# Performance work log

Hardware: AMD Instinct MI355X
Metric: run time of the kernel (lower is better)

Reference implementation:

```python
import jax, jax.numpy as jnp
import numpy as np
from jax import lax

V, E, H, T = 50000, 256, 512, 16  # vocab, embed_dim, hidden_dim, num_tags
B, S = 32, 512
C = 128          # conv channels
HD = H // 2      # per-direction LSTM hidden


def setup_inputs() -> dict:
    key = jax.random.key(0)
    ks = jax.random.split(key, 20)
    g = lambda k, shape, s=0.05: jax.random.normal(k, shape, jnp.float32) * s
    return {
        "x": jax.random.randint(ks[0], (B, S), 0, V),
        "mask": jnp.ones((B, S), jnp.int32),
        "tags": jax.random.randint(ks[1], (B, S), 0, T),
        "embed_table": g(ks[2], (V, E), 0.1),
        "conv_w": g(ks[3], (C, E, 3)),
        "conv_b": g(ks[4], (C,)),
        "wih_f": g(ks[5], (4 * HD, C)),
        "whh_f": g(ks[6], (4 * HD, HD)),
        "bih_f": g(ks[7], (4 * HD,)),
        "bhh_f": g(ks[8], (4 * HD,)),
        "wih_b": g(ks[9], (4 * HD, C)),
        "whh_b": g(ks[10], (4 * HD, HD)),
        "bih_b": g(ks[11], (4 * HD,)),
        "bhh_b": g(ks[12], (4 * HD,)),
        "fc_w": g(ks[13], (T, H)),
        "fc_b": g(ks[14], (T,)),
        "start_trans": g(ks[15], (T,), 0.1),
        "end_trans": g(ks[16], (T,), 0.1),
        "trans": g(ks[17], (T, T), 0.1),
    }


def _lstm_dir(xs, wih, whh, bih, bhh, reverse):
    # xs: [S, B, D] -> hidden states [S, B, HD], PyTorch gate order i,f,g,o
    b = xs.shape[1]
    h0 = jnp.zeros((b, whh.shape[1]), xs.dtype)

    def step(carry, xt):
        h, c = carry
        gates = xt @ wih.T + h @ whh.T + bih + bhh  # [B, 4*HD]
        i, f, g, o = jnp.split(gates, 4, axis=-1)
        c = jax.nn.sigmoid(f) * c + jax.nn.sigmoid(i) * jnp.tanh(g)
        h = jax.nn.sigmoid(o) * jnp.tanh(c)
        return (h, c), h

    _, hs = lax.scan(step, (h0, h0), xs, reverse=reverse)
    return hs


def _crf_nll(emissions, tg, m, start_trans, end_trans, trans):
    # emissions [S,B,T], tg [S,B] int, m [S,B] float -> per-seq -loglik mean
    bidx = jnp.arange(emissions.shape[1])
    # numerator: score of the gold path
    score = start_trans[tg[0]] + emissions[0, bidx, tg[0]]

    def num_step(s, inp):
        prev_t, cur_t, em, mi = inp
        return s + (trans[prev_t, cur_t] + em[bidx, cur_t]) * mi, None

    score, _ = lax.scan(num_step, score, (tg[:-1], tg[1:], emissions[1:], m[1:]))
    seq_ends = m.sum(0).astype(jnp.int32) - 1
    score = score + end_trans[tg[seq_ends, bidx]]
    # denominator: forward algorithm (log partition)
    alpha = start_trans + emissions[0]  # [B,T]

    def den_step(a, inp):
        em, mi = inp
        nxt = jax.nn.logsumexp(a[:, :, None] + trans[None] + em[:, None, :], axis=1)
        return jnp.where(mi[:, None] > 0, nxt, a), None

    alpha, _ = lax.scan(den_step, alpha, (emissions[1:], m[1:]))
    logz = jax.nn.logsumexp(alpha + end_trans[None], axis=1)
    return -jnp.mean(score - logz)


def reference(x, mask, tags, embed_table, conv_w, conv_b, wih_f, whh_f, bih_f,
              bhh_f, wih_b, whh_b, bih_b, bhh_b, fc_w, fc_b, start_trans,
              end_trans, trans):
    emb = embed_table[x]                       # [B,S,E]
    xc = jnp.transpose(emb, (0, 2, 1))         # [B,E,S]
    conv = lax.conv_general_dilated(xc, conv_w, (1,), [(1, 1)],
                                    dimension_numbers=("NCH", "OIH", "NCH"))
    feat = jax.nn.relu(conv + conv_b[None, :, None])   # [B,C,S]
    xs = jnp.transpose(feat, (2, 0, 1))        # [S,B,C]
    hf = _lstm_dir(xs, wih_f, whh_f, bih_f, bhh_f, False)
    hb = _lstm_dir(xs, wih_b, whh_b, bih_b, bhh_b, True)
    h = jnp.concatenate([hf, hb], axis=-1)     # [S,B,H]
    emissions = h @ fc_w.T + fc_b              # [S,B,T]
    m = jnp.transpose(mask, (1, 0)).astype(emissions.dtype)
    tg = jnp.transpose(tags, (1, 0))
    return _crf_nll(emissions, tg, m, start_trans, end_trans, trans)
```

## Files before the change

### kernel.cpp

```cpp
#include <hip/hip_runtime.h>
#include <hip/hip_bf16.h>

constexpr int NB = 32, NS = 512, NE = 256, NC = 128, NHD = 256, NG = 1024, NT = 16, NH = 512;

typedef float f32x4 __attribute__((ext_vector_type(4)));
typedef short bf16x8 __attribute__((ext_vector_type(8)));

__device__ __forceinline__ unsigned short f2bf(float f) {
    unsigned u = __float_as_uint(f);
    u += 0x7fffu + ((u >> 16) & 1u);
    return (unsigned short)(u >> 16);
}
__device__ __forceinline__ float bf2f(unsigned short s) {
    return __uint_as_float(((unsigned)s) << 16);
}
__device__ __forceinline__ float vexp2(float x) {
    float r; asm("v_exp_f32 %0, %1" : "=v"(r) : "v"(x)); return r;
}
__device__ __forceinline__ float vrcp(float x) {
    float r; asm("v_rcp_f32 %0, %1" : "=v"(r) : "v"(x)); return r;
}
__device__ __forceinline__ float vlog2(float x) {
    float r; asm("v_log_f32 %0, %1" : "=v"(r) : "v"(x)); return r;
}
__device__ __forceinline__ unsigned char f2fp8(float v) {
    int r = __builtin_amdgcn_cvt_pk_fp8_f32(v, 0.f, 0, false);
    return (unsigned char)(r & 0xff);
}
__device__ __constant__ float KSC[4] = {-1.442695041f, -1.442695041f, 2.885390082f, -1.442695041f};

__global__ void k_prep_convw(const float* __restrict__ w, float* __restrict__ wT) {
    int i = blockIdx.x * 256 + threadIdx.x;
    if (i >= 768 * 128) return;
    int e3 = i >> 7, c = i & 127;
    wT[i] = w[c * 768 + e3];
}

__global__ void k_prep_scale(const float* __restrict__ whh_f, const float* __restrict__ whh_b,
                             float* __restrict__ scale) {
    int d = blockIdx.y;
    const float* src = d ? whh_b : whh_f;
    int col = blockIdx.x * 256 + threadIdx.x;
    if (col >= 1024) return;
    int j = col >> 2, g = col & 3;
    const float* p = src + (size_t)(g * 256 + j) * 256;
    float m = 0.f;
    for (int k = 0; k < 256; ++k) m = fmaxf(m, fabsf(p[k]));
    scale[d * 1024 + col] = (m > 0.f) ? (m * (1.f / 448.f)) : 1.f;
}

__global__ void k_prep_whh_frag8(const float* __restrict__ whh_f, const float* __restrict__ whh_b,
                                 const float* __restrict__ scale, unsigned char* __restrict__ whhF8) {
    int i = blockIdx.x * 256 + threadIdx.x;
    if (i >= (1 << 19)) return;
    int e = i & 7;
    int lane = (i >> 3) & 63;
    int g = (i >> 9) & 3;
    int kt = (i >> 11) & 7;
    int w = (i >> 14) & 15;
    int d = (i >> 18) & 1;
    const float* src = d ? whh_b : whh_f;
    int j = w * 16 + (lane & 15);
    int k = kt * 32 + (lane >> 4) * 8 + e;
    float sc = scale[d * 1024 + j * 4 + g];
    float v = src[(g * 256 + j) * 256 + k] / sc;
    whhF8[i] = f2fp8(v);
}

__global__ void k_prep_wih_frag(const float* __restrict__ wih_f, const float* __restrict__ wih_b,
                                unsigned short* __restrict__ wihF) {
    int i = blockIdx.x * 256 + threadIdx.x;
    if (i >= (1 << 18)) return;
    int e = i & 7;
    int lane = (i >> 3) & 63;
    int kt = (i >> 9) & 3;
    int ctg = (i >> 11) & 63;
    int d = (i >> 17) & 1;
    const float* src = d ? wih_b : wih_f;
    int row = lane & 15;
    int cell = ctg * 4 + (row >> 2), g = row & 3;
    int k = kt * 32 + (lane >> 4) * 8 + e;
    wihF[i] = f2bf(src[(g * 256 + cell) * 128 + k] * KSC[g]);
}

__global__ void k_prep_bias(const float* __restrict__ bih_f, const float* __restrict__ bhh_f,
                            const float* __restrict__ bih_b, const float* __restrict__ bhh_b,
                            float* __restrict__ bias2s) {
    int d = blockIdx.y;
    const float* bi = d ? bih_b : bih_f;
    const float* bh = d ? bhh_b : bhh_f;
    int i = blockIdx.x * 256 + threadIdx.x;
    if (i >= NG) return;
    int g = i & 3, j = i >> 2;
    bias2s[(size_t)d * NG + i] = (bi[g * 256 + j] + bh[g * 256 + j]) * KSC[g];
}

__global__ __launch_bounds__(128) void k_conv(const int* __restrict__ x,
                                              const float* __restrict__ table,
                                              const float* __restrict__ wT,
                                              const float* __restrict__ conv_b,
                                              unsigned short* __restrict__ feat) {
    int b = blockIdx.y;
    int s0 = blockIdx.x * 8;
    int c = threadIdx.x;
    __shared__ float win[10][NE];
    for (int i = 0; i < 10; ++i) {
        int s = s0 - 1 + i;
        if (s < 0 || s >= NS) {
            for (int e = c; e < NE; e += 128) win[i][e] = 0.f;
        } else {
            int tok = x[b * NS + s];
            const float* row = table + (size_t)tok * NE;
            for (int e = c; e < NE; e += 128) win[i][e] = row[e];
        }
    }
    __syncthreads();
    float acc[8];
    float bc = conv_b[c];
#pragma unroll
    for (int p = 0; p < 8; ++p) acc[p] = bc;
    for (int e = 0; e < NE; ++e) {
        float r[10];
#pragma unroll
        for (int i = 0; i < 10; ++i) r[i] = win[i][e];
#pragma unroll
        for (int k = 0; k < 3; ++k) {
            float wv = wT[(e * 3 + k) * NC + c];
#pragma unroll
            for (int p = 0; p < 8; ++p) acc[p] += wv * r[p + k];
        }
    }
#pragma unroll
    for (int p = 0; p < 8; ++p) {
        feat[((size_t)b * NS + s0 + p) * NC + c] = f2bf(fmaxf(acc[p], 0.f));
    }
}

__global__ __launch_bounds__(256) void k_xgate(const unsigned short* __restrict__ feat,
                                               const unsigned short* __restrict__ wihF,
                                               const float* __restrict__ bias2s,
                                               unsigned short* __restrict__ xg) {
    int d = blockIdx.y;
    int p0 = blockIdx.x * 16;
    int tid = threadIdx.x;
    int w = tid >> 6, l = tid & 63;
    int l15 = l & 15, lq = l >> 4;
    int p = p0 + l15, b = p & 31, s = p >> 5;
    const unsigned short* fp = feat + ((size_t)b * NS + s) * NC + lq * 8;
    bf16x8 bf[4];
#pragma unroll
    for (int kt = 0; kt < 4; ++kt) bf[kt] = *(const bf16x8*)(fp + kt * 32);
    const unsigned short* WF = wihF + ((size_t)d << 17);
    unsigned short* XGD = xg + (size_t)d * NS * NB * NG;
#pragma unroll
    for (int ct = 0; ct < 16; ++ct) {
        int ctg = w * 16 + ct;
        int cell = ctg * 4 + lq;
        float4 bv = *(const float4*)(bias2s + (size_t)d * NG + cell * 4);
        f32x4 acc = {bv.x, bv.y, bv.z, bv.w};
#pragma unroll
        for (int kt = 0; kt < 4; ++kt) {
            bf16x8 af = *(const bf16x8*)(WF + (((size_t)ctg * 4 + kt) * 64 + l) * 8);
            acc = __builtin_amdgcn_mfma_f32_16x16x32_bf16(af, bf[kt], acc, 0, 0, 0);
        }
        unsigned long long hp = (unsigned long long)f2bf(acc[0])
                              | ((unsigned long long)f2bf(acc[1]) << 16)
                              | ((unsigned long long)f2bf(acc[2]) << 32)
                              | ((unsigned long long)f2bf(acc[3]) << 48);
        *(unsigned long long*)(XGD + (size_t)p * 1024 + cell * 4) = hp;
    }
}

__global__ __launch_bounds__(1024, 1) void k_lstm2(const unsigned char* __restrict__ whhF8,
                                                   const float* __restrict__ scale,
                                                   const unsigned short* __restrict__ xg,
                                                   unsigned short* __restrict__ hcat) {
    int bid = blockIdx.x;
    int d = bid >> 1, bh = bid & 1;
    int tid = threadIdx.x;
    int w = tid >> 6, l = tid & 63;
    int l15 = l & 15, lq = l >> 4;
    __shared__ unsigned char hbuf[2][16][280];
    for (int i = tid; i < 2 * 16 * 280; i += 1024) (&hbuf[0][0][0])[i] = 0;
    unsigned long long wf[32];
    const unsigned char* wp = whhF8 + ((size_t)(d * 16 + w) << 14) + (size_t)l * 8;
#pragma unroll
    for (int f = 0; f < 32; ++f) wf[f] = *(const unsigned long long*)(wp + f * 512);
    int cell = w * 16 + l15;
    float csc[4];
#pragma unroll
    for (int g = 0; g < 4; ++g)
        csc[g] = scale[d * 1024 + cell * 4 + g] * KSC[g];
    const unsigned short* XG = xg + (size_t)d * NS * NB * NG;
    float cst[4] = {};
    __syncthreads();
    int cur = 0;
    unsigned long long xq[4];
    {
        int s0 = d ? (NS - 1) : 0;
#pragma unroll
        for (int r = 0; r < 4; ++r)
            xq[r] = *(const unsigned long long*)(
                XG + (size_t)(s0 * 32 + bh * 16 + lq * 4 + r) * 1024 + cell * 4);
    }
    for (int step = 0; step < NS; ++step) {
        int s = d ? (NS - 1 - step) : step;
        unsigned long long xn[4];
        {
            int stn = (step + 1 < NS) ? step + 1 : step;
            int sn = d ? (NS - 1 - stn) : stn;
#pragma unroll
            for (int r = 0; r < 4; ++r)
                xn[r] = *(const unsigned long long*)(
                    XG + (size_t)(sn * 32 + bh * 16 + lq * 4 + r) * 1024 + cell * 4);
        }
        f32x4 acc[4];
#pragma unroll
        for (int g = 0; g < 4; ++g) acc[g] = (f32x4){0.f, 0.f, 0.f, 0.f};
#pragma unroll
        for (int kt = 0; kt < 8; ++kt) {
            unsigned long long a = *(const unsigned long long*)&hbuf[cur][l15][kt * 32 + lq * 8];
#pragma unroll
            for (int g = 0; g < 4; ++g)
                acc[g] = __builtin_amdgcn_mfma_f32_16x16x32_fp8_fp8(
                    (long long)a, (long long)wf[kt * 4 + g], acc[g], 0, 0, 0);
        }
        int nxt = cur ^ 1;
#pragma unroll
        for (int r = 0; r < 4; ++r) {
            unsigned long long xv = xq[r];
            float pi = fmaf(acc[0][r], csc[0], bf2f((unsigned short)xv));
            float pf = fmaf(acc[1][r], csc[1], bf2f((unsigned short)(xv >> 16)));
            float pg = fmaf(acc[2][r], csc[2], bf2f((unsigned short)(xv >> 32)));
            float po = fmaf(acc[3][r], csc[3], bf2f((unsigned short)(xv >> 48)));
            float si = vrcp(1.f + vexp2(pi));
            float sf = vrcp(1.f + vexp2(pf));
            float tg = fmaf(-2.f, vrcp(1.f + vexp2(pg)), 1.f);
            float so = vrcp(1.f + vexp2(po));
            float c = fmaf(sf, cst[r], si * tg);
            cst[r] = c;
            float tc = fmaf(-2.f, vrcp(1.f + vexp2(2.885390082f * c)), 1.f);
            float h = so * tc;
            int b = lq * 4 + r;
            __builtin_nontemporal_store(f2bf(h),
                hcat + (size_t)(s * 32 + bh * 16 + b) * NH + d * NHD + cell);
            hbuf[nxt][b][cell] = f2fp8(h);
        }
        __syncthreads();
        cur = nxt;
#pragma unroll
        for (int r = 0; r < 4; ++r) xq[r] = xn[r];
    }
}

__global__ __launch_bounds__(256) void k_fc(const unsigned short* __restrict__ hcat,
                                            const float* __restrict__ fc_w,
                                            const float* __restrict__ fc_b,
                                            float* __restrict__ em) {
    int p0 = blockIdx.x * 16;
    __shared__ float hv[16][NH];
    for (int i = threadIdx.x; i < 16 * NH; i += 256) {
        int p = i >> 9, hh = i & 511;
        hv[p][hh] = bf2f(hcat[(size_t)(p0 + p) * NH + hh]);
    }
    __syncthreads();
    int p = threadIdx.x >> 4, t = threadIdx.x & 15;
    const float* fw = fc_w + t * NH;
    float acc = fc_b[t];
#pragma unroll 8
    for (int hh = 0; hh < NH; ++hh) acc += hv[p][hh] * fw[hh];
    em[(size_t)(p0 + p) * NT + t] = acc;
}

__global__ __launch_bounds__(64) void k_crf(const float* __restrict__ em,
                                            const int* __restrict__ tags,
                                            const int* __restrict__ mask,
                                            const float* __restrict__ start_t,
                                            const float* __restrict__ end_t,
                                            const float* __restrict__ trans,
                                            float* __restrict__ res) {
    int b = blockIdx.x;
    int tid = threadIdx.x;
    __shared__ float em_sh[NS * NT];
    __shared__ float tr[NT * NT];
    __shared__ float alpha_sh[NT];
    __shared__ float msk[NS];
    __shared__ float sc_sh;
    for (int i = tid; i < NT * NT; i += 64) tr[i] = trans[i];
    for (int i = tid; i < NS * NT; i += 64) {
        int s = i >> 4, t = i & 15;
        em_sh[i] = em[((size_t)s * NB + b) * NT + t];
    }
    for (int s = tid; s < NS; s += 64) msk[s] = (float)mask[b * NS + s];
    __syncthreads();
    float part = 0.f, msum = 0.f;
    for (int s = tid; s < NS; s += 64) msum += msk[s];
    for (int s = 1 + tid; s < NS; s += 64) {
        int pv = tags[b * NS + s - 1], cu = tags[b * NS + s];
        part += (tr[pv * NT + cu] + em_sh[s * NT + cu]) * msk[s];
    }
#pragma unroll
    for (int o = 32; o > 0; o >>= 1) {
        part += __shfl_down(part, o);
        msum += __shfl_down(msum, o);
    }
    if (tid == 0) {
        int t0 = tags[b * NS];
        int send = (int)msum - 1;
        sc_sh = start_t[t0] + em_sh[t0] + part + end_t[tags[b * NS + send]];
    }
    if (tid < NT) alpha_sh[tid] = start_t[tid] + em_sh[tid];
    __syncthreads();
    int t_to = tid >> 2, q = tid & 3;
    for (int s = 1; s < NS; ++s) {
        float v0 = alpha_sh[q * 4 + 0] + tr[(q * 4 + 0) * NT + t_to];
        float v1 = alpha_sh[q * 4 + 1] + tr[(q * 4 + 1) * NT + t_to];
        float v2 = alpha_sh[q * 4 + 2] + tr[(q * 4 + 2) * NT + t_to];
        float v3 = alpha_sh[q * 4 + 3] + tr[(q * 4 + 3) * NT + t_to];
        float mx = fmaxf(fmaxf(v0, v1), fmaxf(v2, v3));
        mx = fmaxf(mx, __shfl_xor(mx, 1));
        mx = fmaxf(mx, __shfl_xor(mx, 2));
        float nmx = -1.442695041f * mx;
        float ss = vexp2(fmaf(v0, 1.442695041f, nmx)) + vexp2(fmaf(v1, 1.442695041f, nmx))
                 + vexp2(fmaf(v2, 1.442695041f, nmx)) + vexp2(fmaf(v3, 1.442695041f, nmx));
        ss += __shfl_xor(ss, 1);
        ss += __shfl_xor(ss, 2);
        float nv = mx + 0.6931471806f * vlog2(ss) + em_sh[s * NT + t_to];
        float old = alpha_sh[t_to];
        nv = (msk[s] > 0.f) ? nv : old;
        __syncthreads();
        if (q == 0) alpha_sh[t_to] = nv;
        __syncthreads();
    }
    if (tid == 0) {
        float mx = -1e30f;
        for (int t = 0; t < NT; ++t) mx = fmaxf(mx, alpha_sh[t] + end_t[t]);
        float sum = 0.f;
        for (int t = 0; t < NT; ++t) sum += vexp2(1.442695041f * (alpha_sh[t] + end_t[t] - mx));
        res[b] = sc_sh - (mx + 0.6931471806f * vlog2(sum));
    }
}

__global__ void k_final(const float* __restrict__ res, float* __restrict__ out) {
    int tid = threadIdx.x;
    float v = (tid < NB) ? res[tid] : 0.f;
#pragma unroll
    for (int o = 32; o > 0; o >>= 1) v += __shfl_down(v, o);
    if (tid == 0) out[0] = -v / NB;
}

constexpr size_t SZ_FEAT  = (size_t)NB * NS * NC * 2;
constexpr size_t SZ_WT    = (size_t)768 * 128 * 4;
constexpr size_t SZ_WHHF8 = (size_t)(1 << 19);
constexpr size_t SZ_SCALE = (size_t)2 * 1024 * 4;
constexpr size_t SZ_WIHF  = (size_t)(1 << 18) * 2;
constexpr size_t SZ_BIAS  = (size_t)2 * NG * 4;
constexpr size_t SZ_XG    = (size_t)2 * NS * NB * NG * 2;
constexpr size_t SZ_HCAT  = (size_t)NS * NB * NH * 2;
constexpr size_t SZ_EM    = (size_t)NS * NB * NT * 4;

constexpr size_t OFF_FEAT  = 0;
constexpr size_t OFF_WT    = OFF_FEAT + SZ_FEAT;
constexpr size_t OFF_WHHF8 = OFF_WT + SZ_WT;
constexpr size_t OFF_SCALE = OFF_WHHF8 + SZ_WHHF8;
constexpr size_t OFF_WIHF  = OFF_SCALE + SZ_SCALE;
constexpr size_t OFF_BIAS  = OFF_WIHF + SZ_WIHF;
constexpr size_t OFF_XG    = OFF_BIAS + SZ_BIAS;
constexpr size_t OFF_HCAT  = OFF_XG + SZ_XG;
constexpr size_t OFF_EM    = OFF_HCAT + SZ_HCAT;
constexpr size_t OFF_RES   = OFF_EM + SZ_EM;

extern "C" void kernel_launch(void* const* d_in, const int* in_sizes, int n_in,
                              void* d_out, int out_size, void* d_ws, size_t ws_size,
                              hipStream_t stream) {
    const int* x        = (const int*)d_in[0];
    const int* mask     = (const int*)d_in[1];
    const int* tags     = (const int*)d_in[2];
    const float* table  = (const float*)d_in[3];
    const float* conv_w = (const float*)d_in[4];
    const float* conv_b = (const float*)d_in[5];
    const float* wih_f  = (const float*)d_in[6];
    const float* whh_f  = (const float*)d_in[7];
    const float* bih_f  = (const float*)d_in[8];
    const float* bhh_f  = (const float*)d_in[9];
    const float* wih_b  = (const float*)d_in[10];
    const float* whh_b  = (const float*)d_in[11];
    const float* bih_b  = (const float*)d_in[12];
    const float* bhh_b  = (const float*)d_in[13];
    const float* fc_w   = (const float*)d_in[14];
    const float* fc_b   = (const float*)d_in[15];
    const float* start_t = (const float*)d_in[16];
    const float* end_t  = (const float*)d_in[17];
    const float* trans  = (const float*)d_in[18];

    char* ws = (char*)d_ws;
    unsigned short* feat = (unsigned short*)(ws + OFF_FEAT);
    float* wT   = (float*)(ws + OFF_WT);
    unsigned char* whhF8 = (unsigned char*)(ws + OFF_WHHF8);
    float* scale = (float*)(ws + OFF_SCALE);
    unsigned short* wihF = (unsigned short*)(ws + OFF_WIHF);
    float* bias2s = (float*)(ws + OFF_BIAS);
    unsigned short* xg = (unsigned short*)(ws + OFF_XG);
    unsigned short* hcat = (unsigned short*)(ws + OFF_HCAT);
    float* em   = (float*)(ws + OFF_EM);
    float* res  = (float*)(ws + OFF_RES);

    k_prep_convw<<<dim3(384), 256, 0, stream>>>(conv_w, wT);
    k_prep_scale<<<dim3(4, 2), 256, 0, stream>>>(whh_f, whh_b, scale);
    k_prep_whh_frag8<<<dim3(2048), 256, 0, stream>>>(whh_f, whh_b, scale, whhF8);
    k_prep_wih_frag<<<dim3(1024), 256, 0, stream>>>(wih_f, wih_b, wihF);
    k_prep_bias<<<dim3(4, 2), 256, 0, stream>>>(bih_f, bhh_f, bih_b, bhh_b, bias2s);
    k_conv<<<dim3(NS / 8, NB), 128, 0, stream>>>(x, table, wT, conv_b, feat);
    k_xgate<<<dim3(NS * NB / 16, 2), 256, 0, stream>>>(feat, wihF, bias2s, xg);
    k_lstm2<<<dim3(4), 1024, 0, stream>>>(whhF8, scale, xg, hcat);
    k_fc<<<dim3(NS * NB / 16), 256, 0, stream>>>(hcat, fc_w, fc_b, em);
    k_crf<<<dim3(NB), 64, 0, stream>>>(em, tags, mask, start_t, end_t, trans, res);
    k_final<<<dim3(1), 64, 0, stream>>>(res, (float*)d_out);
}
```

Before: 1.351 ms.

## Fuse prep kernels, double xgate positions per block, unroll LSTM step loop

Merges four weight-preparation kernels into one launch that dispatches on block index, which cuts kernel launch overhead. Makes each xgate block compute 32 positions instead of 16, so every loaded W_ih fragment feeds two MFMAs. Unrolls the serial LSTM recurrence by two with compile-time LDS buffer indices and incrementally advanced pointers, which removes per-step address arithmetic and dynamic buffer selection. The final prefetch reads one step past the direction's range but stays inside the xg buffer; the extra unrolling may raise register pressure.

```diff
diff --git a/kernel.cpp b/kernel.cpp
--- a/kernel.cpp
+++ b/kernel.cpp
@@ -28,13 +28,6 @@
     return (unsigned char)(r & 0xff);
 }
 __device__ __constant__ float KSC[4] = {-1.442695041f, -1.442695041f, 2.885390082f, -1.442695041f};
-
-__global__ void k_prep_convw(const float* __restrict__ w, float* __restrict__ wT) {
-    int i = blockIdx.x * 256 + threadIdx.x;
-    if (i >= 768 * 128) return;
-    int e3 = i >> 7, c = i & 127;
-    wT[i] = w[c * 768 + e3];
-}
 
 __global__ void k_prep_scale(const float* __restrict__ whh_f, const float* __restrict__ whh_b,
                              float* __restrict__ scale) {
@@ -49,50 +42,55 @@
     scale[d * 1024 + col] = (m > 0.f) ? (m * (1.f / 448.f)) : 1.f;
 }
 
-__global__ void k_prep_whh_frag8(const float* __restrict__ whh_f, const float* __restrict__ whh_b,
-                                 const float* __restrict__ scale, unsigned char* __restrict__ whhF8) {
-    int i = blockIdx.x * 256 + threadIdx.x;
-    if (i >= (1 << 19)) return;
-    int e = i & 7;
-    int lane = (i >> 3) & 63;
-    int g = (i >> 9) & 3;
-    int kt = (i >> 11) & 7;
-    int w = (i >> 14) & 15;
-    int d = (i >> 18) & 1;
-    const float* src = d ? whh_b : whh_f;
-    int j = w * 16 + (lane & 15);
-    int k = kt * 32 + (lane >> 4) * 8 + e;
-    float sc = scale[d * 1024 + j * 4 + g];
-    float v = src[(g * 256 + j) * 256 + k] / sc;
-    whhF8[i] = f2fp8(v);
-}
-
-__global__ void k_prep_wih_frag(const float* __restrict__ wih_f, const float* __restrict__ wih_b,
-                                unsigned short* __restrict__ wihF) {
-    int i = blockIdx.x * 256 + threadIdx.x;
-    if (i >= (1 << 18)) return;
-    int e = i & 7;
-    int lane = (i >> 3) & 63;
-    int kt = (i >> 9) & 3;
-    int ctg = (i >> 11) & 63;
-    int d = (i >> 17) & 1;
-    const float* src = d ? wih_b : wih_f;
-    int row = lane & 15;
-    int cell = ctg * 4 + (row >> 2), g = row & 3;
-    int k = kt * 32 + (lane >> 4) * 8 + e;
-    wihF[i] = f2bf(src[(g * 256 + cell) * 128 + k] * KSC[g]);
-}
-
-__global__ void k_prep_bias(const float* __restrict__ bih_f, const float* __restrict__ bhh_f,
+__global__ void k_prep_main(const float* __restrict__ conv_w, float* __restrict__ wT,
+                            const float* __restrict__ whh_f, const float* __restrict__ whh_b,
+                            const float* __restrict__ scale, unsigned char* __restrict__ whhF8,
+                            const float* __restrict__ wih_f, const float* __restrict__ wih_b,
+                            unsigned short* __restrict__ wihF,
+                            const float* __restrict__ bih_f, const float* __restrict__ bhh_f,
                             const float* __restrict__ bih_b, const float* __restrict__ bhh_b,
                             float* __restrict__ bias2s) {
-    int d = blockIdx.y;
-    const float* bi = d ? bih_b : bih_f;
-    const float* bh = d ? bhh_b : bhh_f;
-    int i = blockIdx.x * 256 + threadIdx.x;
-    if (i >= NG) return;
-    int g = i & 3, j = i >> 2;
-    bias2s[(size_t)d * NG + i] = (bi[g * 256 + j] + bh[g * 256 + j]) * KSC[g];
+    int blk = blockIdx.x;
+    if (blk < 384) {
+        int i = blk * 256 + threadIdx.x;
+        if (i < 768 * 128) {
+            int e3 = i >> 7, c = i & 127;
+            wT[i] = conv_w[c * 768 + e3];
+        }
+    } else if (blk < 2432) {
+        int i = (blk - 384) * 256 + threadIdx.x;
+        int e = i & 7;
+        int lane = (i >> 3) & 63;
+        int g = (i >> 9) & 3;
+        int kt = (i >> 11) & 7;
+        int w = (i >> 14) & 15;
+        int d = (i >> 18) & 1;
+        const float* src = d ? whh_b : whh_f;
+        int j = w * 16 + (lane & 15);
+        int k = kt * 32 + (lane >> 4) * 8 + e;
+        float sc = scale[d * 1024 + j * 4 + g];
+        whhF8[i] = f2fp8(src[(g * 256 + j) * 256 + k] / sc);
+    } else if (blk < 3456) {
+        int i = (blk - 2432) * 256 + threadIdx.x;
+        int e = i & 7;
+        int lane = (i >> 3) & 63;
+        int kt = (i >> 9) & 3;
+        int ctg = (i >> 11) & 63;
+        int d = (i >> 17) & 1;
+        const float* src = d ? wih_b : wih_f;
+        int row = lane & 15;
+        int cell = ctg * 4 + (row >> 2), g = row & 3;
+        int k = kt * 32 + (lane >> 4) * 8 + e;
+        wihF[i] = f2bf(src[(g * 256 + cell) * 128 + k] * KSC[g]);
+    } else {
+        int i = (blk - 3456) * 256 + threadIdx.x;
+        int d = i >> 10;
+        int col = i & 1023;
+        const float* bi = d ? bih_b : bih_f;
+        const float* bh = d ? bhh_b : bhh_f;
+        int g = col & 3, j = col >> 2;
+        bias2s[(size_t)d * NG + col] = (bi[g * 256 + j] + bh[g * 256 + j]) * KSC[g];
+    }
 }
 
 __global__ __launch_bounds__(128) void k_conv(const int* __restrict__ x,
@@ -141,15 +139,21 @@
                                                const float* __restrict__ bias2s,
                                                unsigned short* __restrict__ xg) {
     int d = blockIdx.y;
-    int p0 = blockIdx.x * 16;
+    int p0 = blockIdx.x * 32;
     int tid = threadIdx.x;
     int w = tid >> 6, l = tid & 63;
     int l15 = l & 15, lq = l >> 4;
-    int p = p0 + l15, b = p & 31, s = p >> 5;
-    const unsigned short* fp = feat + ((size_t)b * NS + s) * NC + lq * 8;
-    bf16x8 bf[4];
-#pragma unroll
-    for (int kt = 0; kt < 4; ++kt) bf[kt] = *(const bf16x8*)(fp + kt * 32);
+    int pA = p0 + l15, pB = p0 + 16 + l15;
+    int bA = pA & 31, sA = pA >> 5;
+    int bB = pB & 31, sB = pB >> 5;
+    const unsigned short* fpA = feat + ((size_t)bA * NS + sA) * NC + lq * 8;
+    const unsigned short* fpB = feat + ((size_t)bB * NS + sB) * NC + lq * 8;
+    bf16x8 bfA[4], bfB[4];
+#pragma unroll
+    for (int kt = 0; kt < 4; ++kt) {
+        bfA[kt] = *(const bf16x8*)(fpA + kt * 32);
+        bfB[kt] = *(const bf16x8*)(fpB + kt * 32);
+    }
     const unsigned short* WF = wihF + ((size_t)d << 17);
     unsigned short* XGD = xg + (size_t)d * NS * NB * NG;
 #pragma unroll
@@ -157,17 +161,24 @@
         int ctg = w * 16 + ct;
         int cell = ctg * 4 + lq;
         float4 bv = *(const float4*)(bias2s + (size_t)d * NG + cell * 4);
-        f32x4 acc = {bv.x, bv.y, bv.z, bv.w};
+        f32x4 accA = {bv.x, bv.y, bv.z, bv.w};
+        f32x4 accB = accA;
 #pragma unroll
         for (int kt = 0; kt < 4; ++kt) {
             bf16x8 af = *(const bf16x8*)(WF + (((size_t)ctg * 4 + kt) * 64 + l) * 8);
-            acc = __builtin_amdgcn_mfma_f32_16x16x32_bf16(af, bf[kt], acc, 0, 0, 0);
+            accA = __builtin_amdgcn_mfma_f32_16x16x32_bf16(af, bfA[kt], accA, 0, 0, 0);
+            accB = __builtin_amdgcn_mfma_f32_16x16x32_bf16(af, bfB[kt], accB, 0, 0, 0);
         }
-        unsigned long long hp = (unsigned long long)f2bf(acc[0])
-                              | ((unsigned long long)f2bf(acc[1]) << 16)
-                              | ((unsigned long long)f2bf(acc[2]) << 32)
-                              | ((unsigned long long)f2bf(acc[3]) << 48);
-        *(unsigned long long*)(XGD + (size_t)p * 1024 + cell * 4) = hp;
+        unsigned long long hA = (unsigned long long)f2bf(accA[0])
+                              | ((unsigned long long)f2bf(accA[1]) << 16)
+                              | ((unsigned long long)f2bf(accA[2]) << 32)
+                              | ((unsigned long long)f2bf(accA[3]) << 48);
+        unsigned long long hB = (unsigned long long)f2bf(accB[0])
+                              | ((unsigned long long)f2bf(accB[1]) << 16)
+                              | ((unsigned long long)f2bf(accB[2]) << 32)
+                              | ((unsigned long long)f2bf(accB[3]) << 48);
+        *(unsigned long long*)(XGD + (size_t)pA * 1024 + cell * 4) = hA;
+        *(unsigned long long*)(XGD + (size_t)pB * 1024 + cell * 4) = hB;
     }
 }
 
@@ -191,66 +202,64 @@
 #pragma unroll
     for (int g = 0; g < 4; ++g)
         csc[g] = scale[d * 1024 + cell * 4 + g] * KSC[g];
-    const unsigned short* XG = xg + (size_t)d * NS * NB * NG;
     float cst[4] = {};
+    int s0 = d ? (NS - 1) : 0;
+    const ptrdiff_t xdlt = d ? -(ptrdiff_t)(32 * 1024) : (ptrdiff_t)(32 * 1024);
+    const ptrdiff_t hdlt = d ? -(ptrdiff_t)(32 * 512) : (ptrdiff_t)(32 * 512);
+    const unsigned short* xpA = xg + (size_t)d * NS * NB * NG
+                              + (size_t)(s0 * 32 + bh * 16 + lq * 4) * 1024 + cell * 4;
+    const unsigned short* xpB = xpA + 2048;
+    unsigned short* hp = hcat + (size_t)(s0 * 32 + bh * 16 + lq * 4) * 512 + d * 256 + cell;
     __syncthreads();
-    int cur = 0;
-    unsigned long long xq[4];
-    {
-        int s0 = d ? (NS - 1) : 0;
-#pragma unroll
-        for (int r = 0; r < 4; ++r)
-            xq[r] = *(const unsigned long long*)(
-                XG + (size_t)(s0 * 32 + bh * 16 + lq * 4 + r) * 1024 + cell * 4);
-    }
-    for (int step = 0; step < NS; ++step) {
-        int s = d ? (NS - 1 - step) : step;
-        unsigned long long xn[4];
-        {
-            int stn = (step + 1 < NS) ? step + 1 : step;
-            int sn = d ? (NS - 1 - stn) : stn;
-#pragma unroll
-            for (int r = 0; r < 4; ++r)
-                xn[r] = *(const unsigned long long*)(
-                    XG + (size_t)(sn * 32 + bh * 16 + lq * 4 + r) * 1024 + cell * 4);
-        }
-        f32x4 acc[4];
-#pragma unroll
-        for (int g = 0; g < 4; ++g) acc[g] = (f32x4){0.f, 0.f, 0.f, 0.f};
-#pragma unroll
-        for (int kt = 0; kt < 8; ++kt) {
-            unsigned long long a = *(const unsigned long long*)&hbuf[cur][l15][kt * 32 + lq * 8];
-#pragma unroll
-            for (int g = 0; g < 4; ++g)
-                acc[g] = __builtin_amdgcn_mfma_f32_16x16x32_fp8_fp8(
-                    (long long)a, (long long)wf[kt * 4 + g], acc[g], 0, 0, 0);
-        }
-        int nxt = cur ^ 1;
-#pragma unroll
-        for (int r = 0; r < 4; ++r) {
-            unsigned long long xv = xq[r];
-            float pi = fmaf(acc[0][r], csc[0], bf2f((unsigned short)xv));
-            float pf = fmaf(acc[1][r], csc[1], bf2f((unsigned short)(xv >> 16)));
-            float pg = fmaf(acc[2][r], csc[2], bf2f((unsigned short)(xv >> 32)));
-            float po = fmaf(acc[3][r], csc[3], bf2f((unsigned short)(xv >> 48)));
-            float si = vrcp(1.f + vexp2(pi));
-            float sf = vrcp(1.f + vexp2(pf));
-            float tg = fmaf(-2.f, vrcp(1.f + vexp2(pg)), 1.f);
-            float so = vrcp(1.f + vexp2(po));
-            float c = fmaf(sf, cst[r], si * tg);
-            cst[r] = c;
-            float tc = fmaf(-2.f, vrcp(1.f + vexp2(2.885390082f * c)), 1.f);
-            float h = so * tc;
-            int b = lq * 4 + r;
-            __builtin_nontemporal_store(f2bf(h),
-                hcat + (size_t)(s * 32 + bh * 16 + b) * NH + d * NHD + cell);
-            hbuf[nxt][b][cell] = f2fp8(h);
-        }
-        __syncthreads();
-        cur = nxt;
-#pragma unroll
-        for (int r = 0; r < 4; ++r) xq[r] = xn[r];
-    }
+    unsigned long long xq0 = *(const unsigned long long*)(xpA);
+    unsigned long long xq1 = *(const unsigned long long*)(xpA + 1024);
+    unsigned long long xq2 = *(const unsigned long long*)(xpB);
+    unsigned long long xq3 = *(const unsigned long long*)(xpB + 1024);
+
+#define LSTM_STEP(CUR, NXT)                                                              \
+    {                                                                                    \
+        unsigned long long xn0 = *(const unsigned long long*)(xpA + xdlt);               \
+        unsigned long long xn1 = *(const unsigned long long*)(xpA + xdlt + 1024);        \
+        unsigned long long xn2 = *(const unsigned long long*)(xpB + xdlt);               \
+        unsigned long long xn3 = *(const unsigned long long*)(xpB + xdlt + 1024);        \
+        f32x4 acc0 = {0.f,0.f,0.f,0.f}, acc1 = acc0, acc2 = acc0, acc3 = acc0;           \
+        _Pragma("unroll")                                                                \
+        for (int kt = 0; kt < 8; ++kt) {                                                 \
+            unsigned long long a =                                                       \
+                *(const unsigned long long*)&hbuf[CUR][l15][kt * 32 + lq * 8];           \
+            acc0 = __builtin_amdgcn_mfma_f32_16x16x32_fp8_fp8((long long)a, (long long)wf[kt*4+0], acc0, 0,0,0); \
+            acc1 = __builtin_amdgcn_mfma_f32_16x16x32_fp8_fp8((long long)a, (long long)wf[kt*4+1], acc1, 0,0,0); \
+            acc2 = __builtin_amdgcn_mfma_f32_16x16x32_fp8_fp8((long long)a, (long long)wf[kt*4+2], acc2, 0,0,0); \
+            acc3 = __builtin_amdgcn_mfma_f32_16x16x32_fp8_fp8((long long)a, (long long)wf[kt*4+3], acc3, 0,0,0); \
+        }                                                                                \
+        _Pragma("unroll")                                                                \
+        for (int r = 0; r < 4; ++r) {                                                    \
+            unsigned long long xv = (r == 0) ? xq0 : (r == 1) ? xq1 : (r == 2) ? xq2 : xq3; \
+            float pi = fmaf(acc0[r], csc[0], bf2f((unsigned short)xv));                  \
+            float pf = fmaf(acc1[r], csc[1], bf2f((unsigned short)(xv >> 16)));          \
+            float pg = fmaf(acc2[r], csc[2], bf2f((unsigned short)(xv >> 32)));          \
+            float po = fmaf(acc3[r], csc[3], bf2f((unsigned short)(xv >> 48)));          \
+            float si = vrcp(1.f + vexp2(pi));                                            \
+            float sf = vrcp(1.f + vexp2(pf));                                            \
+            float tg = fmaf(-2.f, vrcp(1.f + vexp2(pg)), 1.f);                           \
+            float so = vrcp(1.f + vexp2(po));                                            \
+            float c = fmaf(sf, cst[r], si * tg);                                         \
+            cst[r] = c;                                                                  \
+            float tc = fmaf(-2.f, vrcp(1.f + vexp2(2.885390082f * c)), 1.f);             \
+            float h = so * tc;                                                           \
+            __builtin_nontemporal_store(f2bf(h), hp + r * 512);                          \
+            hbuf[NXT][lq * 4 + r][cell] = f2fp8(h);                                      \
+        }                                                                                \
+        __syncthreads();                                                                 \
+        xq0 = xn0; xq1 = xn1; xq2 = xn2; xq3 = xn3;                                      \
+        xpA += xdlt; xpB += xdlt; hp += hdlt;                                            \
+    }
+
+    for (int it = 0; it < NS / 2; ++it) {
+        LSTM_STEP(0, 1)
+        LSTM_STEP(1, 0)
+    }
+#undef LSTM_STEP
 }
 
 __global__ __launch_bounds__(256) void k_fc(const unsigned short* __restrict__ hcat,
@@ -405,13 +414,12 @@
     float* em   = (float*)(ws + OFF_EM);
     float* res  = (float*)(ws + OFF_RES);
 
-    k_prep_convw<<<dim3(384), 256, 0, stream>>>(conv_w, wT);
     k_prep_scale<<<dim3(4, 2), 256, 0, stream>>>(whh_f, whh_b, scale);
-    k_prep_whh_frag8<<<dim3(2048), 256, 0, stream>>>(whh_f, whh_b, scale, whhF8);
-    k_prep_wih_frag<<<dim3(1024), 256, 0, stream>>>(wih_f, wih_b, wihF);
-    k_prep_bias<<<dim3(4, 2), 256, 0, stream>>>(bih_f, bhh_f, bih_b, bhh_b, bias2s);
+    k_prep_main<<<dim3(3464), 256, 0, stream>>>(conv_w, wT, whh_f, whh_b, scale, whhF8,
+                                                wih_f, wih_b, wihF,
+                                                bih_f, bhh_f, bih_b, bhh_b, bias2s);
     k_conv<<<dim3(NS / 8, NB), 128, 0, stream>>>(x, table, wT, conv_b, feat);
-    k_xgate<<<dim3(NS * NB / 16, 2), 256, 0, stream>>>(feat, wihF, bias2s, xg);
+    k_xgate<<<dim3(NS * NB / 32, 2), 256, 0, stream>>>(feat, wihF, bias2s, xg);
     k_lstm2<<<dim3(4), 1024, 0, stream>>>(whhF8, scale, xg, hcat);
     k_fc<<<dim3(NS * NB / 16), 256, 0, stream>>>(hcat, fc_w, fc_b, em);
     k_crf<<<dim3(NB), 64, 0, stream>>>(em, tags, mask, start_t, end_t, trans, res);
```

After: 1.397 ms. 1.03x slower.

## Use MX fp8 16x16x128 MFMA in LSTM recurrence, fuse prep kernels, widen xgate tiles

Applied to the files above, without the earlier changes.

The LSTM recurrent matmul switches from eight K=32 fp8 MFMAs per gate to two K=128 scaled MFMAs (gfx950 f8f6f4 builtin), with unit scales and a repacked fp8 weight fragment layout. The four weight-prep kernels are merged into one launch to cut launch overhead. The input-gate kernel now processes 32 positions per block, reusing each weight fragment across two MFMAs. The MX path depends on the builtin being available and on the new fragment layout matching the operand mapping the hardware expects.

```diff
diff --git a/kernel.cpp b/kernel.cpp
--- a/kernel.cpp
+++ b/kernel.cpp
@@ -5,6 +5,14 @@
 
 typedef float f32x4 __attribute__((ext_vector_type(4)));
 typedef short bf16x8 __attribute__((ext_vector_type(8)));
+typedef int i32x8 __attribute__((ext_vector_type(8)));
+typedef unsigned long long u64x4 __attribute__((ext_vector_type(4)));
+
+#if __has_builtin(__builtin_amdgcn_mfma_scale_f32_16x16x128_f8f6f4)
+#define USE_MX 1
+#else
+#define USE_MX 0
+#endif
 
 __device__ __forceinline__ unsigned short f2bf(float f) {
     unsigned u = __float_as_uint(f);
@@ -28,13 +36,6 @@
     return (unsigned char)(r & 0xff);
 }
 __device__ __constant__ float KSC[4] = {-1.442695041f, -1.442695041f, 2.885390082f, -1.442695041f};
-
-__global__ void k_prep_convw(const float* __restrict__ w, float* __restrict__ wT) {
-    int i = blockIdx.x * 256 + threadIdx.x;
-    if (i >= 768 * 128) return;
-    int e3 = i >> 7, c = i & 127;
-    wT[i] = w[c * 768 + e3];
-}
 
 __global__ void k_prep_scale(const float* __restrict__ whh_f, const float* __restrict__ whh_b,
                              float* __restrict__ scale) {
@@ -49,50 +50,69 @@
     scale[d * 1024 + col] = (m > 0.f) ? (m * (1.f / 448.f)) : 1.f;
 }
 
-__global__ void k_prep_whh_frag8(const float* __restrict__ whh_f, const float* __restrict__ whh_b,
-                                 const float* __restrict__ scale, unsigned char* __restrict__ whhF8) {
-    int i = blockIdx.x * 256 + threadIdx.x;
-    if (i >= (1 << 19)) return;
-    int e = i & 7;
-    int lane = (i >> 3) & 63;
-    int g = (i >> 9) & 3;
-    int kt = (i >> 11) & 7;
-    int w = (i >> 14) & 15;
-    int d = (i >> 18) & 1;
-    const float* src = d ? whh_b : whh_f;
-    int j = w * 16 + (lane & 15);
-    int k = kt * 32 + (lane >> 4) * 8 + e;
-    float sc = scale[d * 1024 + j * 4 + g];
-    float v = src[(g * 256 + j) * 256 + k] / sc;
-    whhF8[i] = f2fp8(v);
-}
-
-__global__ void k_prep_wih_frag(const float* __restrict__ wih_f, const float* __restrict__ wih_b,
-                                unsigned short* __restrict__ wihF) {
-    int i = blockIdx.x * 256 + threadIdx.x;
-    if (i >= (1 << 18)) return;
-    int e = i & 7;
-    int lane = (i >> 3) & 63;
-    int kt = (i >> 9) & 3;
-    int ctg = (i >> 11) & 63;
-    int d = (i >> 17) & 1;
-    const float* src = d ? wih_b : wih_f;
-    int row = lane & 15;
-    int cell = ctg * 4 + (row >> 2), g = row & 3;
-    int k = kt * 32 + (lane >> 4) * 8 + e;
-    wihF[i] = f2bf(src[(g * 256 + cell) * 128 + k] * KSC[g]);
-}
-
-__global__ void k_prep_bias(const float* __restrict__ bih_f, const float* __restrict__ bhh_f,
+__global__ void k_prep_main(const float* __restrict__ conv_w, float* __restrict__ wT,
+                            const float* __restrict__ whh_f, const float* __restrict__ whh_b,
+                            const float* __restrict__ scale, unsigned char* __restrict__ whhF8,
+                            const float* __restrict__ wih_f, const float* __restrict__ wih_b,
+                            unsigned short* __restrict__ wihF,
+                            const float* __restrict__ bih_f, const float* __restrict__ bhh_f,
                             const float* __restrict__ bih_b, const float* __restrict__ bhh_b,
                             float* __restrict__ bias2s) {
-    int d = blockIdx.y;
-    const float* bi = d ? bih_b : bih_f;
-    const float* bh = d ? bhh_b : bhh_f;
-    int i = blockIdx.x * 256 + threadIdx.x;
-    if (i >= NG) return;
-    int g = i & 3, j = i >> 2;
-    bias2s[(size_t)d * NG + i] = (bi[g * 256 + j] + bh[g * 256 + j]) * KSC[g];
+    int blk = blockIdx.x;
+    if (blk < 384) {
+        int i = blk * 256 + threadIdx.x;
+        if (i < 768 * 128) {
+            int e3 = i >> 7, c = i & 127;
+            wT[i] = conv_w[c * 768 + e3];
+        }
+    } else if (blk < 2432) {
+        int i = (blk - 384) * 256 + threadIdx.x;
+#if USE_MX
+        int e = i & 31;
+        int lane = (i >> 5) & 63;
+        int frag = (i >> 11) & 7;
+        int w = (i >> 14) & 15;
+        int d = (i >> 18) & 1;
+        int g = frag >> 1, n = frag & 1;
+        const float* src = d ? whh_b : whh_f;
+        int j = w * 16 + (lane & 15);
+        int k = n * 128 + ((lane >> 4) & 3) * 32 + e;
+        float sc = scale[d * 1024 + j * 4 + g];
+        whhF8[i] = f2fp8(src[(g * 256 + j) * 256 + k] / sc);
+#else
+        int e = i & 7;
+        int lane = (i >> 3) & 63;
+        int g = (i >> 9) & 3;
+        int kt = (i >> 11) & 7;
+        int w = (i >> 14) & 15;
+        int d = (i >> 18) & 1;
+        const float* src = d ? whh_b : whh_f;
+        int j = w * 16 + (lane & 15);
+        int k = kt * 32 + (lane >> 4) * 8 + e;
+        float sc = scale[d * 1024 + j * 4 + g];
+        whhF8[i] = f2fp8(src[(g * 256 + j) * 256 + k] / sc);
+#endif
+    } else if (blk < 3456) {
+        int i = (blk - 2432) * 256 + threadIdx.x;
+        int e = i & 7;
+        int lane = (i >> 3) & 63;
+        int kt = (i >> 9) & 3;
+        int ctg = (i >> 11) & 63;
+        int d = (i >> 17) & 1;
+        const float* src = d ? wih_b : wih_f;
+        int row = lane & 15;
+        int cell = ctg * 4 + (row >> 2), g = row & 3;
+        int k = kt * 32 + (lane >> 4) * 8 + e;
+        wihF[i] = f2bf(src[(g * 256 + cell) * 128 + k] * KSC[g]);
+    } else {
+        int i = (blk - 3456) * 256 + threadIdx.x;
+        int d = i >> 10;
+        int col = i & 1023;
+        const float* bi = d ? bih_b : bih_f;
+        const float* bh = d ? bhh_b : bhh_f;
+        int g = col & 3, j = col >> 2;
+        bias2s[(size_t)d * NG + col] = (bi[g * 256 + j] + bh[g * 256 + j]) * KSC[g];
+    }
 }
 
 __global__ __launch_bounds__(128) void k_conv(const int* __restrict__ x,
@@ -141,15 +161,21 @@
                                                const float* __restrict__ bias2s,
                                                unsigned short* __restrict__ xg) {
     int d = blockIdx.y;
-    int p0 = blockIdx.x * 16;
+    int p0 = blockIdx.x * 32;
     int tid = threadIdx.x;
     int w = tid >> 6, l = tid & 63;
     int l15 = l & 15, lq = l >> 4;
-    int p = p0 + l15, b = p & 31, s = p >> 5;
-    const unsigned short* fp = feat + ((size_t)b * NS + s) * NC + lq * 8;
-    bf16x8 bf[4];
-#pragma unroll
-    for (int kt = 0; kt < 4; ++kt) bf[kt] = *(const bf16x8*)(fp + kt * 32);
+    int pA = p0 + l15, pB = p0 + 16 + l15;
+    int bA = pA & 31, sA = pA >> 5;
+    int bB = pB & 31, sB = pB >> 5;
+    const unsigned short* fpA = feat + ((size_t)bA * NS + sA) * NC + lq * 8;
+    const unsigned short* fpB = feat + ((size_t)bB * NS + sB) * NC + lq * 8;
+    bf16x8 bfA[4], bfB[4];
+#pragma unroll
+    for (int kt = 0; kt < 4; ++kt) {
+        bfA[kt] = *(const bf16x8*)(fpA + kt * 32);
+        bfB[kt] = *(const bf16x8*)(fpB + kt * 32);
+    }
     const unsigned short* WF = wihF + ((size_t)d << 17);
     unsigned short* XGD = xg + (size_t)d * NS * NB * NG;
 #pragma unroll
@@ -157,17 +183,24 @@
         int ctg = w * 16 + ct;
         int cell = ctg * 4 + lq;
         float4 bv = *(const float4*)(bias2s + (size_t)d * NG + cell * 4);
-        f32x4 acc = {bv.x, bv.y, bv.z, bv.w};
+        f32x4 accA = {bv.x, bv.y, bv.z, bv.w};
+        f32x4 accB = accA;
 #pragma unroll
         for (int kt = 0; kt < 4; ++kt) {
             bf16x8 af = *(const bf16x8*)(WF + (((size_t)ctg * 4 + kt) * 64 + l) * 8);
-            acc = __builtin_amdgcn_mfma_f32_16x16x32_bf16(af, bf[kt], acc, 0, 0, 0);
-        }
-        unsigned long long hp = (unsigned long long)f2bf(acc[0])
-                              | ((unsigned long long)f2bf(acc[1]) << 16)
-                              | ((unsigned long long)f2bf(acc[2]) << 32)
-                              | ((unsigned long long)f2bf(acc[3]) << 48);
-        *(unsigned long long*)(XGD + (size_t)p * 1024 + cell * 4) = hp;
+            accA = __builtin_amdgcn_mfma_f32_16x16x32_bf16(af, bfA[kt], accA, 0, 0, 0);
+            accB = __builtin_amdgcn_mfma_f32_16x16x32_bf16(af, bfB[kt], accB, 0, 0, 0);
+        }
+        unsigned long long hA = (unsigned long long)f2bf(accA[0])
+                              | ((unsigned long long)f2bf(accA[1]) << 16)
+                              | ((unsigned long long)f2bf(accA[2]) << 32)
+                              | ((unsigned long long)f2bf(accA[3]) << 48);
+        unsigned long long hB = (unsigned long long)f2bf(accB[0])
+                              | ((unsigned long long)f2bf(accB[1]) << 16)
+                              | ((unsigned long long)f2bf(accB[2]) << 32)
+                              | ((unsigned long long)f2bf(accB[3]) << 48);
+        *(unsigned long long*)(XGD + (size_t)pA * 1024 + cell * 4) = hA;
+        *(unsigned long long*)(XGD + (size_t)pB * 1024 + cell * 4) = hB;
     }
 }
 
@@ -182,10 +215,21 @@
     int l15 = l & 15, lq = l >> 4;
     __shared__ unsigned char hbuf[2][16][280];
     for (int i = tid; i < 2 * 16 * 280; i += 1024) (&hbuf[0][0][0])[i] = 0;
+#if USE_MX
+    i32x8 wf8[8];
+    {
+        const unsigned char* wp = whhF8 + ((size_t)(d * 16 + w) << 14) + (size_t)l * 32;
+#pragma unroll
+        for (int f = 0; f < 8; ++f) wf8[f] = *(const i32x8*)(wp + f * 2048);
+    }
+#else
     unsigned long long wf[32];
-    const unsigned char* wp = whhF8 + ((size_t)(d * 16 + w) << 14) + (size_t)l * 8;
-#pragma unroll
-    for (int f = 0; f < 32; ++f) wf[f] = *(const unsigned long long*)(wp + f * 512);
+    {
+        const unsigned char* wp = whhF8 + ((size_t)(d * 16 + w) << 14) + (size_t)l * 8;
+#pragma unroll
+        for (int f = 0; f < 32; ++f) wf[f] = *(const unsigned long long*)(wp + f * 512);
+    }
+#endif
     int cell = w * 16 + l15;
     float csc[4];
 #pragma unroll
@@ -217,6 +261,26 @@
         f32x4 acc[4];
 #pragma unroll
         for (int g = 0; g < 4; ++g) acc[g] = (f32x4){0.f, 0.f, 0.f, 0.f};
+#if USE_MX
+        {
+            const unsigned char* hrow = &hbuf[cur][l15][0];
+#pragma unroll
+            for (int n = 0; n < 2; ++n) {
+                int base = n * 128 + lq * 32;
+                u64x4 t;
+                t[0] = *(const unsigned long long*)(hrow + base);
+                t[1] = *(const unsigned long long*)(hrow + base + 8);
+                t[2] = *(const unsigned long long*)(hrow + base + 16);
+                t[3] = *(const unsigned long long*)(hrow + base + 24);
+                i32x8 av = __builtin_bit_cast(i32x8, t);
+#pragma unroll
+                for (int g = 0; g < 4; ++g)
+                    acc[g] = __builtin_amdgcn_mfma_scale_f32_16x16x128_f8f6f4(
+                        av, wf8[g * 2 + n], acc[g], 0, 0,
+                        0, 0x7f7f7f7f, 0, 0x7f7f7f7f);
+            }
+        }
+#else
 #pragma unroll
         for (int kt = 0; kt < 8; ++kt) {
             unsigned long long a = *(const unsigned long long*)&hbuf[cur][l15][kt * 32 + lq * 8];
@@ -225,6 +289,7 @@
                 acc[g] = __builtin_amdgcn_mfma_f32_16x16x32_fp8_fp8(
                     (long long)a, (long long)wf[kt * 4 + g], acc[g], 0, 0, 0);
         }
+#endif
         int nxt = cur ^ 1;
 #pragma unroll
         for (int r = 0; r < 4; ++r) {
@@ -405,13 +470,12 @@
     float* em   = (float*)(ws + OFF_EM);
     float* res  = (float*)(ws + OFF_RES);
 
-    k_prep_convw<<<dim3(384), 256, 0, stream>>>(conv_w, wT);
     k_prep_scale<<<dim3(4, 2), 256, 0, stream>>>(whh_f, whh_b, scale);
-    k_prep_whh_frag8<<<dim3(2048), 256, 0, stream>>>(whh_f, whh_b, scale, whhF8);
-    k_prep_wih_frag<<<dim3(1024), 256, 0, stream>>>(wih_f, wih_b, wihF);
-    k_prep_bias<<<dim3(4, 2), 256, 0, stream>>>(bih_f, bhh_f, bih_b, bhh_b, bias2s);
+    k_prep_main<<<dim3(3464), 256, 0, stream>>>(conv_w, wT, whh_f, whh_b, scale, whhF8,
+                                                wih_f, wih_b, wihF,
+                                                bih_f, bhh_f, bih_b, bhh_b, bias2s);
     k_conv<<<dim3(NS / 8, NB), 128, 0, stream>>>(x, table, wT, conv_b, feat);
-    k_xgate<<<dim3(NS * NB / 16, 2), 256, 0, stream>>>(feat, wihF, bias2s, xg);
+    k_xgate<<<dim3(NS * NB / 32, 2), 256, 0, stream>>>(feat, wihF, bias2s, xg);
     k_lstm2<<<dim3(4), 1024, 0, stream>>>(whhF8, scale, xg, hcat);
     k_fc<<<dim3(NS * NB / 16), 256, 0, stream>>>(hcat, fc_w, fc_b, em);
     k_crf<<<dim3(NB), 64, 0, stream>>>(em, tags, mask, start_t, end_t, trans, res);
```

After: 1.895 ms. 40.2% more time.
